# Optimization experiments

Measured on AMD Instinct MI355X. Metric: run time of the kernel, lower is better.

Reference implementation:

```python
import jax, jax.numpy as jnp
import numpy as np
import math

NUM_HEADS = 16
HEAD_DIM = 128
NUM_KV_HEADS = 4
SCALE = 1.0 / math.sqrt(HEAD_DIM)
NEG_INF = -1e30


def setup_inputs() -> dict:
    key = jax.random.key(0)
    k1, k2, k3 = jax.random.split(key, 3)
    total_tokens = 8192  # batch=4 sequences of uniform length 2048, packed
    q = jax.random.normal(k1, (total_tokens, NUM_HEADS * HEAD_DIM), dtype=jnp.float32)
    k = jax.random.normal(k2, (total_tokens, NUM_KV_HEADS * HEAD_DIM), dtype=jnp.float32)
    v = jax.random.normal(k3, (total_tokens, NUM_KV_HEADS * HEAD_DIM), dtype=jnp.float32)
    return {"q": q, "k": k, "v": v, "seq_len": 2048}


def reference(q, k, v, seq_len):
    # Varlen prefill attention with uniform per-sequence lengths ==
    # cu_seqlens = [0, S, 2S, ...]; equivalent to the per-sequence loop in
    # flash_attn_varlen_func, vectorized over the batch dimension.
    T = q.shape[0]
    B = T // seq_len
    G = NUM_HEADS // NUM_KV_HEADS  # queries per kv head (GQA)
    # [B, S, Hkv, G, D] / [B, S, Hkv, D]
    qh = q.reshape(B, seq_len, NUM_KV_HEADS, G, HEAD_DIM)
    kh = k.reshape(B, seq_len, NUM_KV_HEADS, HEAD_DIM)
    vh = v.reshape(B, seq_len, NUM_KV_HEADS, HEAD_DIM)
    # GQA without materializing repeated K/V: contract each query group
    # against its shared kv head (same math as repeat_interleave + SDPA).
    scores = jnp.einsum('bqhgd,bkhd->bhgqk', qh, kh) * SCALE
    causal = jnp.tril(jnp.ones((seq_len, seq_len), dtype=bool))
    scores = jnp.where(causal, scores, NEG_INF)
    probs = jax.nn.softmax(scores, axis=-1)
    out = jnp.einsum('bhgqk,bkhd->bqhgd', probs, vh)
    return out.reshape(T, NUM_HEADS * HEAD_DIM)
```

## Files before the change

### kernel.cpp

```cpp
#include <hip/hip_runtime.h>
#include <hip/hip_bf16.h>
#include <stdint.h>

#define NH    16
#define HKVN  4
#define D     128
#define SEQ   2048
#define BATCH 4
#define QTILE 128
#define KVC   64

#define SCALE_LOG2E 0.12751741f
#define THR 11.0f

typedef __attribute__((ext_vector_type(4)))  float    f32x4;
typedef __attribute__((ext_vector_type(16))) float    f32x16;
typedef __attribute__((ext_vector_type(8)))  short    s16x8;
typedef __attribute__((ext_vector_type(4)))  short    s16x4;
typedef __attribute__((ext_vector_type(4)))  uint32_t u32x4;
typedef __attribute__((ext_vector_type(8)))  __bf16   bf16x8;

__device__ __forceinline__ uint32_t cvt_pk(float lo, float hi) {
  uint32_t r;
  asm("v_cvt_pk_bf16_f32 %0, %1, %2" : "=v"(r) : "v"(lo), "v"(hi));
  return r;
}
__device__ __forceinline__ void pswap(uint32_t& a, uint32_t& b) {
  auto r = __builtin_amdgcn_permlane32_swap(a, b, false, false);
  a = r[0];
  b = r[1];
}
__device__ __forceinline__ float cross_max(float x) {
  uint32_t a = __builtin_bit_cast(uint32_t, x), b = a;
  pswap(a, b);
  return fmaxf(__builtin_bit_cast(float, a), __builtin_bit_cast(float, b));
}
__device__ __forceinline__ float cross_sum(float x) {
  uint32_t a = __builtin_bit_cast(uint32_t, x), b = a;
  pswap(a, b);
  return __builtin_bit_cast(float, a) + __builtin_bit_cast(float, b);
}
__device__ __forceinline__ f32x16 mfma32(s16x8 a, s16x8 b, f32x16 c) {
  return __builtin_amdgcn_mfma_f32_32x32x16_bf16(
      __builtin_bit_cast(bf16x8, a), __builtin_bit_cast(bf16x8, b), c, 0, 0, 0);
}

__global__ __launch_bounds__(256, 2) void attn_fwd(
    const float* __restrict__ Q, const float* __restrict__ K,
    const float* __restrict__ V, float* __restrict__ O) {
  __shared__ __align__(16) short KT[2][KVC * D];
  __shared__ __align__(16) short VT[2][KVC * D];

  const int bid = blockIdx.x;
  const int grp = bid >> 8;
  const int i   = bid & 255;
  const int s   = i & 3;
  int qt;
  switch (grp) { case 0: qt = 15 - s; break; case 1: qt = s; break;
                 case 2: qt = 11 - s; break; default: qt = 4 + s; }
  const int bh  = i >> 2;
  const int b   = bh >> 4;
  const int hq  = bh & 15;
  const int hkv = hq >> 2;

  const int tid  = threadIdx.x;
  const int wq   = tid >> 6;
  const int lane = tid & 63;
  const int l31  = lane & 31;
  const int h2   = lane >> 5;
  const int h16  = (lane >> 4) & 1;
  const int l15  = lane & 15;

  const int q0   = qt * QTILE;
  const int qg   = q0 + wq * 32 + l31;
  const int qmin = q0 + wq * 32;
  const int qmax = qmin + 31;
  const int nch  = 2 * qt + 2;

  const float* qp = Q + (size_t)(b * SEQ + qg) * (NH * D) + hq * D;
  s16x8 qf[8];
#pragma unroll
  for (int kb = 0; kb < 8; ++kb) {
    f32x4 x0 = *(const f32x4*)(qp + kb * 16 + h2 * 8);
    f32x4 x1 = *(const f32x4*)(qp + kb * 16 + h2 * 8 + 4);
    u32x4 w;
    w[0] = cvt_pk(x0[0] * SCALE_LOG2E, x0[1] * SCALE_LOG2E);
    w[1] = cvt_pk(x0[2] * SCALE_LOG2E, x0[3] * SCALE_LOG2E);
    w[2] = cvt_pk(x1[0] * SCALE_LOG2E, x1[1] * SCALE_LOG2E);
    w[3] = cvt_pk(x1[2] * SCALE_LOG2E, x1[3] * SCALE_LOG2E);
    qf[kb] = __builtin_bit_cast(s16x8, w);
  }

  f32x16 acc[4];
#pragma unroll
  for (int dt = 0; dt < 4; ++dt)
#pragma unroll
    for (int r = 0; r < 16; ++r) acc[dt][r] = 0.f;
  float m_r = -1e30f, l_r = 0.f;

  const float* Kg = K + (size_t)b * SEQ * (HKVN * D) + hkv * D;
  const float* Vg = V + (size_t)b * SEQ * (HKVN * D) + hkv * D;

  const int srow = tid >> 2;
  const int scol = (tid & 3) * 32;

  f32x4 kl[8], vl[8];
#define STAGE_LOADS(kvb_) do {                                               \
    const float* kr_ = Kg + (size_t)((kvb_) + srow) * (HKVN * D) + scol;     \
    const float* vr_ = Vg + (size_t)((kvb_) + srow) * (HKVN * D) + scol;     \
    _Pragma("unroll") for (int u = 0; u < 8; ++u)                            \
      kl[u] = *(const f32x4*)(kr_ + u * 4);                                  \
    _Pragma("unroll") for (int u = 0; u < 8; ++u)                            \
      vl[u] = *(const f32x4*)(vr_ + u * 4);                                  \
  } while (0)

#define STAGE_WRITES(nbuf_) do {                                             \
    short* kd_ = &KT[nbuf_][srow * D];                                       \
    short* vd_ = &VT[nbuf_][0];                                              \
    _Pragma("unroll") for (int g = 0; g < 4; ++g) {                          \
      u32x4 wk_, wv_;                                                        \
      wk_[0] = cvt_pk(kl[2*g][0], kl[2*g][1]);                               \
      wk_[1] = cvt_pk(kl[2*g][2], kl[2*g][3]);                               \
      wk_[2] = cvt_pk(kl[2*g+1][0], kl[2*g+1][1]);                           \
      wk_[3] = cvt_pk(kl[2*g+1][2], kl[2*g+1][3]);                           \
      wv_[0] = cvt_pk(vl[2*g][0], vl[2*g][1]);                               \
      wv_[1] = cvt_pk(vl[2*g][2], vl[2*g][3]);                               \
      wv_[2] = cvt_pk(vl[2*g+1][0], vl[2*g+1][1]);                           \
      wv_[3] = cvt_pk(vl[2*g+1][2], vl[2*g+1][3]);                           \
      *(u32x4*)(kd_ + ((scol + g * 8) ^ ((srow & 7) * 8))) = wk_;            \
      const int d_ = scol + g * 8;                                           \
      *(u32x4*)(vd_ + ((srow >> 2) * 8 + (d_ >> 4)) * 64 +                   \
                (srow & 3) * 16 + (d_ & 15)) = wv_;                          \
    }                                                                        \
  } while (0)

  STAGE_LOADS(0);
  STAGE_WRITES(0);
  __syncthreads();

  for (int c = 0; c < nch; ++c) {
    const int cur = c & 1, nxt = cur ^ 1;
    const int kvb = c * KVC;
    const bool have_next = (c + 1 < nch);
    const bool active = (kvb <= qmax);

    if (have_next) {
      STAGE_LOADS(kvb + KVC);
      __builtin_amdgcn_sched_barrier(0);
    }

    f32x16 st[2];
    s16x8 pf[4];
    if (active) {
#pragma unroll
      for (int t = 0; t < 2; ++t) {
#pragma unroll
        for (int r = 0; r < 16; ++r) st[t][r] = 0.f;
        const int row = t * 32 + l31;
        const short* rp = &KT[cur][row * D];
        const int sw = (row & 7) * 8;
#pragma unroll
        for (int kb = 0; kb < 8; ++kb) {
          s16x8 kf = *(const s16x8*)(rp + ((kb * 16 + h2 * 8) ^ sw));
          st[t] = mfma32(kf, qf[kb], st[t]);
        }
      }
      if (kvb + 63 > qmin) {
#pragma unroll
        for (int t = 0; t < 2; ++t)
#pragma unroll
          for (int r = 0; r < 16; ++r) {
            const int kv = kvb + t * 32 + (r & 3) + 8 * (r >> 2) + 4 * h2;
            if (kv > qg) st[t][r] = -1e30f;
          }
      }
      float pm = st[0][0];
#pragma unroll
      for (int t = 0; t < 2; ++t)
#pragma unroll
        for (int r = 0; r < 16; ++r) pm = fmaxf(pm, st[t][r]);
      const float pmax = cross_max(pm);
      if (__any(pmax > m_r + THR)) {
        const float mn = fmaxf(m_r, pmax);
        const float al = __builtin_amdgcn_exp2f(m_r - mn);
        m_r = mn;
        l_r *= al;
#pragma unroll
        for (int dt = 0; dt < 4; ++dt)
#pragma unroll
          for (int r = 0; r < 16; ++r) acc[dt][r] *= al;
      }
      float p[32];
      float rs = 0.f;
#pragma unroll
      for (int t = 0; t < 2; ++t)
#pragma unroll
        for (int r = 0; r < 16; ++r) {
          const float e = __builtin_amdgcn_exp2f(st[t][r] - m_r);
          p[t * 16 + r] = e;
          rs += e;
        }
      l_r += cross_sum(rs);
#pragma unroll
      for (int ks = 0; ks < 4; ++ks) {
        const int o = (ks >> 1) * 16 + (ks & 1) * 8;
        uint32_t A0 = cvt_pk(p[o + 0], p[o + 1]);
        uint32_t A1 = cvt_pk(p[o + 2], p[o + 3]);
        uint32_t B0 = cvt_pk(p[o + 4], p[o + 5]);
        uint32_t B1 = cvt_pk(p[o + 6], p[o + 7]);
        pswap(A0, B0);
        pswap(A1, B1);
        u32x4 w; w[0] = A0; w[1] = A1; w[2] = B0; w[3] = B1;
        pf[ks] = __builtin_bit_cast(s16x8, w);
      }
    }

    if (have_next) {
      STAGE_WRITES(nxt);
    }

    if (active) {
      const uint32_t vbase = (uint32_t)(uintptr_t)&VT[cur][0];
#pragma unroll
      for (int dt = 0; dt < 4; ++dt) {
        s16x4 a0[4], a1[4];
#pragma unroll
        for (int ks = 0; ks < 4; ++ks) {
          const uint32_t ad =
              vbase + (uint32_t)((((ks * 4 + h2 * 2) * 8 + 2 * dt + h16) * 64 +
                                  l15 * 4) * 2);
          asm volatile("ds_read_b64_tr_b16 %0, %2\n\t"
                       "ds_read_b64_tr_b16 %1, %2 offset:1024"
                       : "=&v"(a0[ks]), "=&v"(a1[ks])
                       : "v"(ad)
                       : "memory");
        }
        asm volatile("s_waitcnt lgkmcnt(0)" ::: "memory");
        __builtin_amdgcn_sched_barrier(0);
#pragma unroll
        for (int ks = 0; ks < 4; ++ks) {
          s16x8 vf = __builtin_shufflevector(a0[ks], a1[ks], 0, 1, 2, 3, 4, 5, 6, 7);
          acc[dt] = mfma32(vf, pf[ks], acc[dt]);
        }
      }
    }
    __syncthreads();
  }

  const float inv = 1.0f / l_r;
  float* op = O + (size_t)(b * SEQ + qg) * (NH * D) + hq * D;
#pragma unroll
  for (int dt = 0; dt < 4; ++dt) {
#pragma unroll
    for (int rg = 0; rg < 4; ++rg) {
      f32x4 o;
      o[0] = acc[dt][rg * 4 + 0] * inv;
      o[1] = acc[dt][rg * 4 + 1] * inv;
      o[2] = acc[dt][rg * 4 + 2] * inv;
      o[3] = acc[dt][rg * 4 + 3] * inv;
      *(f32x4*)(op + dt * 32 + rg * 8 + h2 * 4) = o;
    }
  }
}

extern "C" void kernel_launch(void* const* d_in, const int* in_sizes, int n_in,
                              void* d_out, int out_size, void* d_ws, size_t ws_size,
                              hipStream_t stream) {
  const float* q = (const float*)d_in[0];
  const float* k = (const float*)d_in[1];
  const float* v = (const float*)d_in[2];
  float* o = (float*)d_out;
  dim3 grid(BATCH * NH * (SEQ / QTILE));
  attn_fwd<<<grid, 256, 0, stream>>>(q, k, v, o);
}
```

Baseline: 279.0 us.

## Single-buffer V, restructure K/V staging schedule and prefetch transposed V reads

Moves V to a single LDS buffer and cuts shared memory, which lets launch bounds ask for 3 blocks per CU. The loop is rescheduled: V is written at the start of each iteration, K for the next chunk after PV, and the syncthreads calls become explicit waitcnt+barrier pairs, two per chunk. The transposed V reads are double-buffered across the dt loop so LDS reads overlap the MFMAs, and s_setprio raises wave priority around the MFMA sections. The risks are more register pressure under the tighter launch bound, which could spill, and an extra barrier per chunk.

```diff
diff --git a/kernel.cpp b/kernel.cpp
--- a/kernel.cpp
+++ b/kernel.cpp
@@ -45,11 +45,11 @@
       __builtin_bit_cast(bf16x8, a), __builtin_bit_cast(bf16x8, b), c, 0, 0, 0);
 }
 
-__global__ __launch_bounds__(256, 2) void attn_fwd(
+__global__ __launch_bounds__(256, 3) void attn_fwd(
     const float* __restrict__ Q, const float* __restrict__ K,
     const float* __restrict__ V, float* __restrict__ O) {
   __shared__ __align__(16) short KT[2][KVC * D];
-  __shared__ __align__(16) short VT[2][KVC * D];
+  __shared__ __align__(16) short VT[KVC * D];
 
   const int bid = blockIdx.x;
   const int grp = bid >> 8;
@@ -103,6 +103,7 @@
 
   const int srow = tid >> 2;
   const int scol = (tid & 3) * 32;
+  const uint32_t vbase = (uint32_t)(uintptr_t)&VT[0];
 
   f32x4 kl[8], vl[8];
 #define STAGE_LOADS(kvb_) do {                                               \
@@ -114,44 +115,74 @@
       vl[u] = *(const f32x4*)(vr_ + u * 4);                                  \
   } while (0)
 
-#define STAGE_WRITES(nbuf_) do {                                             \
+#define K_WRITE(nbuf_) do {                                                  \
     short* kd_ = &KT[nbuf_][srow * D];                                       \
-    short* vd_ = &VT[nbuf_][0];                                              \
     _Pragma("unroll") for (int g = 0; g < 4; ++g) {                          \
-      u32x4 wk_, wv_;                                                        \
+      u32x4 wk_;                                                             \
       wk_[0] = cvt_pk(kl[2*g][0], kl[2*g][1]);                               \
       wk_[1] = cvt_pk(kl[2*g][2], kl[2*g][3]);                               \
       wk_[2] = cvt_pk(kl[2*g+1][0], kl[2*g+1][1]);                           \
       wk_[3] = cvt_pk(kl[2*g+1][2], kl[2*g+1][3]);                           \
+      *(u32x4*)(kd_ + ((scol + g * 8) ^ ((srow & 7) * 8))) = wk_;            \
+    }                                                                        \
+  } while (0)
+
+#define V_WRITE() do {                                                       \
+    _Pragma("unroll") for (int g = 0; g < 4; ++g) {                          \
+      u32x4 wv_;                                                             \
       wv_[0] = cvt_pk(vl[2*g][0], vl[2*g][1]);                               \
       wv_[1] = cvt_pk(vl[2*g][2], vl[2*g][3]);                               \
       wv_[2] = cvt_pk(vl[2*g+1][0], vl[2*g+1][1]);                           \
       wv_[3] = cvt_pk(vl[2*g+1][2], vl[2*g+1][3]);                           \
-      *(u32x4*)(kd_ + ((scol + g * 8) ^ ((srow & 7) * 8))) = wk_;            \
       const int d_ = scol + g * 8;                                           \
-      *(u32x4*)(vd_ + ((srow >> 2) * 8 + (d_ >> 4)) * 64 +                   \
+      *(u32x4*)(&VT[0] + ((srow >> 2) * 8 + (d_ >> 4)) * 64 +                \
                 (srow & 3) * 16 + (d_ & 15)) = wv_;                          \
     }                                                                        \
   } while (0)
 
+#define TR_ISSUE(dt_, sl_) do {                                              \
+    _Pragma("unroll") for (int ks = 0; ks < 4; ++ks) {                       \
+      const uint32_t ad_ = vbase +                                           \
+          (uint32_t)((((ks * 4 + h2 * 2) * 8 + 2 * (dt_) + h16) * 64 +       \
+                      l15 * 4) * 2);                                         \
+      asm volatile("ds_read_b64_tr_b16 %0, %2\n\t"                           \
+                   "ds_read_b64_tr_b16 %1, %2 offset:1024"                   \
+                   : "=&v"(ta[sl_][ks]), "=&v"(tb[sl_][ks])                  \
+                   : "v"(ad_)                                                \
+                   : "memory");                                              \
+    }                                                                        \
+  } while (0)
+
+#define LGKM_BAR() do {                                                      \
+    asm volatile("s_waitcnt lgkmcnt(0)" ::: "memory");                       \
+    __builtin_amdgcn_s_barrier();                                            \
+  } while (0)
+
   STAGE_LOADS(0);
-  STAGE_WRITES(0);
-  __syncthreads();
+  K_WRITE(0);
+  V_WRITE();
+  if (nch > 1) STAGE_LOADS(KVC);
+  LGKM_BAR();
 
   for (int c = 0; c < nch; ++c) {
-    const int cur = c & 1, nxt = cur ^ 1;
+    const int cur = c & 1;
     const int kvb = c * KVC;
     const bool have_next = (c + 1 < nch);
     const bool active = (kvb <= qmax);
 
-    if (have_next) {
-      STAGE_LOADS(kvb + KVC);
-      __builtin_amdgcn_sched_barrier(0);
+    if (c > 0) {
+      V_WRITE();
+      if (have_next) {
+        STAGE_LOADS(kvb + KVC);
+        __builtin_amdgcn_sched_barrier(0);
+      }
     }
 
     f32x16 st[2];
     s16x8 pf[4];
+    s16x4 ta[2][4], tb[2][4];
     if (active) {
+      __builtin_amdgcn_s_setprio(1);
 #pragma unroll
       for (int t = 0; t < 2; ++t) {
 #pragma unroll
@@ -165,6 +196,14 @@
           st[t] = mfma32(kf, qf[kb], st[t]);
         }
       }
+      __builtin_amdgcn_s_setprio(0);
+    }
+
+    LGKM_BAR();
+
+    if (active) {
+      TR_ISSUE(0, 0);
+
       if (kvb + 63 > qmin) {
 #pragma unroll
         for (int t = 0; t < 2; ++t)
@@ -213,38 +252,29 @@
         u32x4 w; w[0] = A0; w[1] = A1; w[2] = B0; w[3] = B1;
         pf[ks] = __builtin_bit_cast(s16x8, w);
       }
-    }
-
-    if (have_next) {
-      STAGE_WRITES(nxt);
-    }
-
-    if (active) {
-      const uint32_t vbase = (uint32_t)(uintptr_t)&VT[cur][0];
+
 #pragma unroll
       for (int dt = 0; dt < 4; ++dt) {
-        s16x4 a0[4], a1[4];
+        if (dt < 3) {
+          TR_ISSUE(dt + 1, (dt + 1) & 1);
+          asm volatile("s_waitcnt lgkmcnt(8)" ::: "memory");
+        } else {
+          asm volatile("s_waitcnt lgkmcnt(0)" ::: "memory");
+        }
+        __builtin_amdgcn_sched_barrier(0);
+        __builtin_amdgcn_s_setprio(1);
 #pragma unroll
         for (int ks = 0; ks < 4; ++ks) {
-          const uint32_t ad =
-              vbase + (uint32_t)((((ks * 4 + h2 * 2) * 8 + 2 * dt + h16) * 64 +
-                                  l15 * 4) * 2);
-          asm volatile("ds_read_b64_tr_b16 %0, %2\n\t"
-                       "ds_read_b64_tr_b16 %1, %2 offset:1024"
-                       : "=&v"(a0[ks]), "=&v"(a1[ks])
-                       : "v"(ad)
-                       : "memory");
-        }
-        asm volatile("s_waitcnt lgkmcnt(0)" ::: "memory");
-        __builtin_amdgcn_sched_barrier(0);
-#pragma unroll
-        for (int ks = 0; ks < 4; ++ks) {
-          s16x8 vf = __builtin_shufflevector(a0[ks], a1[ks], 0, 1, 2, 3, 4, 5, 6, 7);
+          s16x8 vf = __builtin_shufflevector(ta[dt & 1][ks], tb[dt & 1][ks],
+                                             0, 1, 2, 3, 4, 5, 6, 7);
           acc[dt] = mfma32(vf, pf[ks], acc[dt]);
         }
+        __builtin_amdgcn_s_setprio(0);
       }
     }
-    __syncthreads();
+
+    if (have_next) K_WRITE(cur ^ 1);
+    LGKM_BAR();
   }
 
   const float inv = 1.0f / l_r;
```

Result: slower. 802.4 us (+187.6%).
